# Optimization experiments

Hardware: AMD Instinct MI355X
Metric: run time of the kernel (lower is better)

The kernel has to match this reference:

```python
import jax, jax.numpy as jnp
import numpy as np

D_MODEL = 2048
N_HEADS = 16
N_KV = 4
D_HEAD = D_MODEL // N_HEADS  # 128
N_REP = N_HEADS // N_KV      # 4
ROPE_BASE = 1000000.0


def _rope_tables(T, d_head, dtype):
    # inv_freq = (1/base)^(2i/d) for i in [0, d/2)
    i = jnp.arange(d_head // 2, dtype=jnp.float32)
    inv_freq = (1.0 / ROPE_BASE) ** (2.0 * i / d_head)
    theta = jnp.arange(T, dtype=jnp.float32)[:, None] * inv_freq[None, :]  # [T, d/2]
    theta = jnp.concatenate([theta, theta], axis=-1)                        # [T, d]
    return jnp.sin(theta).astype(dtype), jnp.cos(theta).astype(dtype)


def _apply_rope(x, sin, cos):
    # x: [B, h, T, d]; sin/cos: [T, d]
    x1, x2 = jnp.split(x, 2, axis=-1)
    rot = jnp.concatenate([-x2, x1], axis=-1)
    return cos[None, None] * x + sin[None, None] * rot


def setup_inputs() -> dict:
    key = jax.random.key(0)
    ks = jax.random.split(key, 9)
    B, T = 2, 2048
    s_in = 1.0 / np.sqrt(D_MODEL)
    return {
        "x": jax.random.normal(ks[0], (B, T, D_MODEL), jnp.float32),
        "wq": jax.random.normal(ks[1], (D_MODEL, N_HEADS * D_HEAD), jnp.float32) * s_in,
        "bq": jax.random.normal(ks[2], (N_HEADS * D_HEAD,), jnp.float32) * 0.02,
        "wk": jax.random.normal(ks[3], (D_MODEL, N_KV * D_HEAD), jnp.float32) * s_in,
        "bk": jax.random.normal(ks[4], (N_KV * D_HEAD,), jnp.float32) * 0.02,
        "wv": jax.random.normal(ks[5], (D_MODEL, N_KV * D_HEAD), jnp.float32) * s_in,
        "bv": jax.random.normal(ks[6], (N_KV * D_HEAD,), jnp.float32) * 0.02,
        "wo": jax.random.normal(ks[7], (D_MODEL, D_MODEL), jnp.float32) * s_in,
    }


def reference(x, wq, bq, wk, bk, wv, bv, wo):
    B, T, C = x.shape
    sin, cos = _rope_tables(T, D_HEAD, x.dtype)

    q = (x @ wq + bq).reshape(B, T, N_HEADS, D_HEAD).transpose(0, 2, 1, 3)  # [B,H,T,d]
    k = (x @ wk + bk).reshape(B, T, N_KV, D_HEAD).transpose(0, 2, 1, 3)     # [B,KV,T,d]
    v = (x @ wv + bv).reshape(B, T, N_KV, D_HEAD).transpose(0, 2, 1, 3)     # [B,KV,T,d]

    q = _apply_rope(q, sin, cos)
    k = _apply_rope(k, sin, cos)

    # GQA: group query heads as [B, KV, rep, T, d] to broadcast against k/v
    qg = q.reshape(B, N_KV, N_REP, T, D_HEAD)
    scale = 1.0 / jnp.sqrt(jnp.asarray(D_HEAD, x.dtype))
    scores = jnp.einsum('bkrqd,bksd->bkrqs', qg, k) * scale  # [B,KV,rep,T,S]

    causal = jnp.tril(jnp.ones((T, T), dtype=bool))
    neg = jnp.asarray(jnp.finfo(x.dtype).min, x.dtype)
    scores = jnp.where(causal[None, None, None], scores, neg)
    p = jax.nn.softmax(scores, axis=-1)

    out = jnp.einsum('bkrqs,bksd->bkrqd', p, v)               # [B,KV,rep,T,d]
    out = out.reshape(B, N_HEADS, T, D_HEAD).transpose(0, 2, 1, 3).reshape(B, T, C)
    return out @ wo, k, v
```

## Files before the change

### kernel.cpp

```cpp
#include <hip/hip_runtime.h>
#include <hip/hip_bf16.h>
#include <math.h>

#define BB 2
#define TT 2048
#define DMODEL 2048
#define NH 16
#define NKV 4
#define DH 128
#define NQKV 3072
#define MM (BB*TT)

typedef unsigned short u16;
typedef unsigned int u32;

typedef __bf16 bf16x8 __attribute__((ext_vector_type(8)));
typedef __bf16 bf16x4 __attribute__((ext_vector_type(4)));
typedef short short4v __attribute__((ext_vector_type(4)));
typedef float f32x4 __attribute__((ext_vector_type(4)));

__device__ __forceinline__ u16 f2b(float f) {
  union { float f; u32 u; } v; v.f = f;
  u32 r = v.u + 0x7fffu + ((v.u >> 16) & 1u);
  return (u16)(r >> 16);
}
__device__ __forceinline__ float b2f(u16 h) {
  union { u32 u; float f; } v; v.u = ((u32)h) << 16;
  return v.f;
}
__device__ __forceinline__ u32 pack2bf(float x, float y) {
  union { float f; u32 u; } a, b; a.f = x; b.f = y;
  return ((a.u + 0x8000u) >> 16) | ((b.u + 0x8000u) & 0xffff0000u);
}

__device__ __forceinline__ void gload16(const void* g, void* l) {
  __builtin_amdgcn_global_load_lds(
      (const __attribute__((address_space(1))) unsigned int*)g,
      (__attribute__((address_space(3))) unsigned int*)l, 16, 0, 0);
}

__device__ __forceinline__ float fast_exp2(float x) {
#if __has_builtin(__builtin_amdgcn_exp2f)
  return __builtin_amdgcn_exp2f(x);
#else
  return __expf(x * 0.6931471805599453f);
#endif
}

__device__ __forceinline__ f32x4 mfma16(bf16x4 a, bf16x4 b, f32x4 c) {
#if __has_builtin(__builtin_amdgcn_mfma_f32_16x16x16bf16_1k)
  union { bf16x4 b; short4v s; } ua, ub;
  ua.b = a; ub.b = b;
  return __builtin_amdgcn_mfma_f32_16x16x16bf16_1k(ua.s, ub.s, c, 0, 0, 0);
#elif __has_builtin(__builtin_amdgcn_mfma_f32_16x16x16_bf16)
  return __builtin_amdgcn_mfma_f32_16x16x16_bf16(a, b, c, 0, 0, 0);
#else
  asm volatile("v_mfma_f32_16x16x16_bf16 %0, %1, %2, %0"
               : "+v"(c) : "v"(a), "v"(b));
  return c;
#endif
}

__global__ void cvt_x_kernel(const float* __restrict__ x, u16* __restrict__ xb, int n4) {
  int i = blockIdx.x * 256 + threadIdx.x;
  if (i < n4) {
    float4 v = ((const float4*)x)[i];
    u32 lo = (u32)f2b(v.x) | ((u32)f2b(v.y) << 16);
    u32 hi = (u32)f2b(v.z) | ((u32)f2b(v.w) << 16);
    uint2 r; r.x = lo; r.y = hi;
    ((uint2*)xb)[i] = r;
  }
}

__global__ void rope_table_kernel(float2* __restrict__ tab) {
  int i = blockIdx.x * 256 + threadIdx.x;
  int t = i >> 6, d = i & 63;
  float inv = exp2f(-(float)d * 0.31143075889569023f);
  float th = (float)t * inv;
  float2 cs; cs.x = cosf(th); cs.y = sinf(th);
  tab[i] = cs;
}

__global__ void transpose_cvt_all_kernel(const float* __restrict__ wq,
                                         const float* __restrict__ wk,
                                         const float* __restrict__ wv,
                                         const float* __restrict__ wo,
                                         u16* __restrict__ wqkvT,
                                         u16* __restrict__ woT) {
  __shared__ u16 t[64][65];
  int bx = blockIdx.x;
  const float* src; u16* dst; int srcCols, rowOff, cb;
  if (bx < 32)      { src = wq; dst = wqkvT; srcCols = 2048; rowOff = 0;    cb = bx; }
  else if (bx < 40) { src = wk; dst = wqkvT; srcCols = 512;  rowOff = 2048; cb = bx - 32; }
  else if (bx < 48) { src = wv; dst = wqkvT; srcCols = 512;  rowOff = 2560; cb = bx - 40; }
  else              { src = wo; dst = woT;   srcCols = 2048; rowOff = 0;    cb = bx - 48; }
  int c0 = cb * 64, r0 = blockIdx.y * 64;
  int tid = threadIdx.x;
  for (int i = tid; i < 4096; i += 256) {
    int r = i >> 6, c = i & 63;
    t[r][c] = f2b(src[(size_t)(r0 + r) * srcCols + c0 + c]);
  }
  __syncthreads();
  for (int i = tid; i < 4096; i += 256) {
    int n = i >> 6, k = i & 63;
    dst[(size_t)(rowOff + c0 + n) * 2048 + r0 + k] = t[k][n];
  }
}


#define BARRIER asm volatile("s_barrier" ::: "memory")
#define LGKM0   asm volatile("s_waitcnt lgkmcnt(0)" ::: "memory")

#define STAGE_A(H, KT, RB) do { \
    const u16* g_ = gA + (size_t)(H) * 262144 + (size_t)(KT) * 64; \
    gload16(g_,          sm + (RB) + tid * 8); \
    gload16(g_ + 131072, sm + (RB) + 4096 + tid * 8); \
  } while (0)

#define STAGE_B(H, KT, RB) do { \
    const u16* g_ = gB + (size_t)(H) * 262144 + (size_t)(KT) * 64; \
    gload16(g_,          sm + (RB) + tid * 8); \
    gload16(g_ + 131072, sm + (RB) + 4096 + tid * 8); \
  } while (0)

#define LDA(BU, MH) do { \
    const u16* ab_ = sm + (BU) + (MH) * 8192 + lra * 64; \
    _Pragma("unroll") \
    for (int mi = 0; mi < 4; mi++) { \
      a[mi][0] = *(const bf16x8*)&ab_[mi * 1024 + as0]; \
      a[mi][1] = *(const bf16x8*)&ab_[mi * 1024 + as1]; \
    } \
  } while (0)

#define LDB(BU, NL) do { \
    const u16* bb_ = sm + (BU) + 16384 + hb * 8192 + lrb * 64; \
    _Pragma("unroll") \
    for (int nj = 0; nj < 2; nj++) { \
      b[(NL)*2+nj][0] = *(const bf16x8*)&bb_[((NL)*2+nj) * 1024 + bs0]; \
      b[(NL)*2+nj][1] = *(const bf16x8*)&bb_[((NL)*2+nj) * 1024 + bs1]; \
    } \
  } while (0)

#define MFMAQ(MH, NL) do { \
    _Pragma("unroll") \
    for (int mi = 0; mi < 4; mi++) \
      _Pragma("unroll") \
      for (int nj = 0; nj < 2; nj++) { \
        acc[(MH)*4+mi][(NL)*2+nj] = __builtin_amdgcn_mfma_f32_16x16x32_bf16( \
            a[mi][0], b[(NL)*2+nj][0], acc[(MH)*4+mi][(NL)*2+nj], 0, 0, 0); \
        acc[(MH)*4+mi][(NL)*2+nj] = __builtin_amdgcn_mfma_f32_16x16x32_bf16( \
            a[mi][1], b[(NL)*2+nj][1], acc[(MH)*4+mi][(NL)*2+nj], 0, 0, 0); \
      } \
  } while (0)

#define TILE4(BU, OBU, KA1, KN) do { \
     \
    LDA(BU, 0); LDB(BU, 0); \
    STAGE_A(1, KA1, (OBU) + 8192); \
    asm volatile("s_waitcnt lgkmcnt(8)" ::: "memory"); \
    BARRIER; LGKM0; \
    __builtin_amdgcn_s_setprio(1); MFMAQ(0, 0); __builtin_amdgcn_s_setprio(0); \
    BARRIER; \
     \
    LDB(BU, 1); \
    STAGE_A(0, KN, (BU)); \
    BARRIER; LGKM0; \
    __builtin_amdgcn_s_setprio(1); MFMAQ(0, 1); __builtin_amdgcn_s_setprio(0); \
    BARRIER; \
     \
    LDA(BU, 1); \
    STAGE_B(0, KN, (BU) + 16384); \
    asm volatile("s_waitcnt lgkmcnt(4)" ::: "memory"); \
    BARRIER; LGKM0; \
    __builtin_amdgcn_s_setprio(1); MFMAQ(1, 1); __builtin_amdgcn_s_setprio(0); \
    BARRIER; \
     \
    STAGE_B(1, KN, (BU) + 24576); \
    BARRIER; LGKM0; \
    __builtin_amdgcn_s_setprio(1); MFMAQ(1, 0); __builtin_amdgcn_s_setprio(0); \
    asm volatile("s_waitcnt vmcnt(6)\n\ts_barrier" ::: "memory"); \
  } while (0)

__global__ __launch_bounds__(512, 2) void gemm_qkv_kernel(
    const u16* __restrict__ A, const u16* __restrict__ Bt,
    const float* __restrict__ bq, const float* __restrict__ bk,
    const float* __restrict__ bv, const float2* __restrict__ rtab,
    u16* __restrict__ qb, u16* __restrict__ kb, u16* __restrict__ vt,
    float* __restrict__ outK, float* __restrict__ outV) {
  __shared__ __align__(16) u16 sm[65536];
  const int tid  = threadIdx.x;
  const int lane = tid & 63;
  const int wave = tid >> 6;
  const int wm   = wave >> 2;
  const int wn   = wave & 3;
  const int quad = lane >> 4;
  const int l16  = lane & 15;
  const int m0 = blockIdx.y * 256;
  const int n0 = blockIdx.x * 256;
  const int bx = blockIdx.x;

  const int srow = tid >> 3;
  const int sch  = (tid & 7) ^ (srow & 7);
  const u16* gA = A  + (size_t)(m0 + srow) * 2048 + sch * 8;
  const u16* gB = Bt + (size_t)(n0 + srow) * 2048 + sch * 8;

  const int lra = wm * 64 + l16;
  const int lrb = (wn & 1) * 64 + l16;
  const int hb  = wn >> 1;
  const int as0 = ((quad)     ^ (lra & 7)) << 3;
  const int as1 = ((quad + 4) ^ (lra & 7)) << 3;
  const int bs0 = ((quad)     ^ (lrb & 7)) << 3;
  const int bs1 = ((quad + 4) ^ (lrb & 7)) << 3;

  bf16x8 a[4][2], b[4][2];
  f32x4 acc[8][4];
  const f32x4 zero = {0.f, 0.f, 0.f, 0.f};
#pragma unroll
  for (int i = 0; i < 8; i++)
#pragma unroll
    for (int j = 0; j < 4; j++) acc[i][j] = zero;

  STAGE_A(0, 0, 0);
  STAGE_B(0, 0, 16384);
  STAGE_B(1, 0, 24576);
  STAGE_A(1, 0, 8192);
  STAGE_A(0, 1, 32768);
  STAGE_B(0, 1, 32768 + 16384);
  STAGE_B(1, 1, 32768 + 24576);
  asm volatile("s_waitcnt vmcnt(6)\n\ts_barrier" ::: "memory");

#pragma unroll 1
  for (int it2 = 0; it2 < 16; ++it2) {
    const int ka1 = (2 * it2 + 1) & 31;
    const int kn0 = (2 * it2 + 2) & 31;
    const int kn1 = (2 * it2 + 3) & 31;
    TILE4(0,     32768, ka1, kn0);
    TILE4(32768, 0,     kn0, kn1);
  }

  asm volatile("s_waitcnt vmcnt(0)\n\ts_barrier" ::: "memory");

  const int cls = (bx < 8) ? 0 : ((bx < 10) ? 1 : 2);
#pragma unroll
  for (int nf = 0; nf < 4; nf++) {
    int col = wn * 64 + nf * 16 + l16;
    int gcol = n0 + col;
    float bval = (cls == 0) ? bq[gcol] : ((cls == 1) ? bk[gcol - 2048] : bv[gcol - 2560]);
#pragma unroll
    for (int mh = 0; mh < 2; mh++)
#pragma unroll
      for (int mi = 0; mi < 4; mi++)
#pragma unroll
        for (int r = 0; r < 4; r++) {
          int row = mh * 128 + wm * 64 + mi * 16 + quad * 4 + r;
          int ci = (row * 256 + col) ^ ((row & 7) << 3);
          sm[ci] = f2b(acc[mh * 4 + mi][nf][r] + bval);
        }
  }
  __syncthreads();

  const int bidx = m0 >> 11;
  const int trow0 = m0 & 2047;

  if (cls < 2) {
    const int isQ = (cls == 0);
#pragma unroll
    for (int itq = 0; itq < 8; itq++) {
      int id = tid + itq * 512;
      int lh = id >> 11;
      int rem = id & 2047;
      int row = rem >> 3, oc = rem & 7;
      int t = trow0 + row;
      int rl = t & 63, ttile = t >> 6;
      int sw = (row & 7) << 3;
      int i0 = (row * 256 + lh * 128 + oc * 8);
      uint4 lo = *(const uint4*)&sm[i0 ^ sw];
      uint4 hi = *(const uint4*)&sm[(i0 + 64) ^ sw];
      const u16* plo = (const u16*)&lo;
      const u16* phi = (const u16*)&hi;
      u16 y1[8], y2[8];
      float f1[8], f2v[8];
#pragma unroll
      for (int j = 0; j < 8; j++) {
        float2 cs = rtab[(t << 6) + oc * 8 + j];
        float x1 = b2f(plo[j]), x2 = b2f(phi[j]);
        f1[j]  = cs.x * x1 - cs.y * x2;
        f2v[j] = cs.x * x2 + cs.y * x1;
        y1[j] = f2b(f1[j]);
        y2[j] = f2b(f2v[j]);
      }
      if (isQ) {
        int hh = bx * 2 + lh;
        size_t tb = ((size_t)(bidx * NH + hh) * 32 + ttile) * 8192;
        *(uint4*)&qb[tb + (size_t)((oc)     * 64 + rl) * 8] = *(const uint4*)y1;
        *(uint4*)&qb[tb + (size_t)((oc + 8) * 64 + rl) * 8] = *(const uint4*)y2;
      } else {
        int hh = bx * 2 + lh - 16;
        size_t tb = ((size_t)(bidx * NKV + hh) * 32 + ttile) * 8192;
        *(uint4*)&kb[tb + (size_t)((oc)     * 64 + rl) * 8] = *(const uint4*)y1;
        *(uint4*)&kb[tb + (size_t)((oc + 8) * 64 + rl) * 8] = *(const uint4*)y2;
        size_t base = ((size_t)(bidx * NKV + hh) * TT + t) * DH + oc * 8;
        *(float4*)&outK[base]          = *(const float4*)&f1[0];
        *(float4*)&outK[base + 4]      = *(const float4*)&f1[4];
        *(float4*)&outK[base + 64]     = *(const float4*)&f2v[0];
        *(float4*)&outK[base + 64 + 4] = *(const float4*)&f2v[4];
      }
    }
  } else {
#pragma unroll
    for (int itv = 0; itv < 16; itv++) {
      int id = tid + itv * 512;
      int lh = id >> 12;
      int rem = id & 4095;
      int row = rem >> 4, oc = rem & 15;
      int kvh = bx * 2 + lh - 20;
      int i0 = (row * 256 + lh * 128 + oc * 8) ^ ((row & 7) << 3);
      uint4 v = *(const uint4*)&sm[i0];
      const u16* pv = (const u16*)&v;
      float f[8];
#pragma unroll
      for (int j = 0; j < 8; j++) f[j] = b2f(pv[j]);
      size_t base = ((size_t)(bidx * NKV + kvh) * TT + trow0 + row) * DH + oc * 8;
      *(float4*)&outV[base]     = *(const float4*)&f[0];
      *(float4*)&outV[base + 4] = *(const float4*)&f[4];
    }
#pragma unroll
    for (int itv = 0; itv < 16; itv++) {
      int id = tid + itv * 512;
      int lh = id >> 12;
      int rem = id & 4095;
      int st = rem >> 10;
      int rem2 = rem & 1023;
      int chunk = rem2 >> 7, dl = rem2 & 127;
      int m = chunk >> 2, qd = chunk & 3;
      int kvh = bx * 2 + lh - 20;
      u16 tmp[8];
#pragma unroll
      for (int e = 0; e < 8; e++) {
        int srw = (2 * m + (e >> 2)) * 16 + qd * 4 + (e & 3);
        int row = st * 64 + srw;
        int idx = (row * 256 + lh * 128 + dl) ^ ((row & 7) << 3);
        tmp[e] = sm[idx];
      }
      int tt = (trow0 >> 6) + st;
      size_t tilebase = ((size_t)(bidx * NKV + kvh) * 32 + tt) * 8192;
      *(uint4*)&vt[tilebase + (size_t)(chunk * 128 + dl) * 8] = *(const uint4*)tmp;
    }
  }
}

__global__ __launch_bounds__(256, 3) void gemm_out_kernel(
    const u16* __restrict__ A, const u16* __restrict__ Bt,
    float* __restrict__ Cout, int M, int N, int K) {
  __shared__ __align__(16) u16 smo[16384];
  const int tid  = threadIdx.x;
  const int lane = tid & 63;
  const int wave = tid >> 6;
  const int quad = lane >> 4;
  const int l16  = lane & 15;
  const int m0 = blockIdx.y * 128;
  const int n0 = blockIdx.x * 128;
  const int wrow = (wave >> 1) * 64;
  const int wcol = (wave & 1) * 64;

  f32x4 acc[4][4];
  const f32x4 zero = {0.f, 0.f, 0.f, 0.f};
#pragma unroll
  for (int i = 0; i < 4; i++)
#pragma unroll
    for (int j = 0; j < 4; j++) acc[i][j] = zero;

  const int srow = tid >> 2;
  const int scol = (tid & 3) * 8;
  const u16* ga = A  + (size_t)(m0 + srow) * K + scol;
  const u16* gb = Bt + (size_t)(n0 + srow) * K + scol;

  gload16(ga,                  &smo[tid * 8]);
  gload16(ga + (size_t)64 * K, &smo[2048 + tid * 8]);
  gload16(gb,                  &smo[4096 + tid * 8]);
  gload16(gb + (size_t)64 * K, &smo[6144 + tid * 8]);

  for (int k0 = 0; k0 < K; k0 += 32) {
    const int p = (k0 >> 5) & 1;
    const int kn = (k0 + 32 == K) ? 0 : k0 + 32;
    u16* nb = &smo[(p ^ 1) * 8192];
    gload16(ga + kn,                  nb + tid * 8);
    gload16(ga + kn + (size_t)64 * K, nb + 2048 + tid * 8);
    gload16(gb + kn,                  nb + 4096 + tid * 8);
    gload16(gb + kn + (size_t)64 * K, nb + 6144 + tid * 8);
    asm volatile("s_waitcnt vmcnt(4)\n\ts_barrier" ::: "memory");
    const u16* cb = &smo[p * 8192];
    bf16x8 af[4], bf[4];
#pragma unroll
    for (int mi = 0; mi < 4; mi++)
      af[mi] = *(const bf16x8*)&cb[(wrow + mi * 16 + l16) * 32 + quad * 8];
#pragma unroll
    for (int ni = 0; ni < 4; ni++)
      bf[ni] = *(const bf16x8*)&cb[4096 + (wcol + ni * 16 + l16) * 32 + quad * 8];
    asm volatile("s_waitcnt lgkmcnt(0)\n\ts_barrier" ::: "memory");
#pragma unroll
    for (int mi = 0; mi < 4; mi++)
#pragma unroll
      for (int ni = 0; ni < 4; ni++)
        acc[mi][ni] = __builtin_amdgcn_mfma_f32_16x16x32_bf16(af[mi], bf[ni], acc[mi][ni], 0, 0, 0);
  }
  asm volatile("s_waitcnt vmcnt(0)" ::: "memory");

#pragma unroll
  for (int ni = 0; ni < 4; ni++) {
    int gcol = n0 + wcol + ni * 16 + l16;
#pragma unroll
    for (int mi = 0; mi < 4; mi++) {
#pragma unroll
      for (int r = 0; r < 4; r++) {
        int grow = m0 + wrow + mi * 16 + quad * 4 + r;
        Cout[(size_t)grow * N + gcol] = acc[mi][ni][r];
      }
    }
  }
}

__global__ __launch_bounds__(256, 2) void attn_kernel(
    const u16* __restrict__ Qt, const u16* __restrict__ Kt,
    const u16* __restrict__ Vt, u16* __restrict__ Ob) {
  __shared__ __align__(16) u16 sm[24576];
  u16* vbuf = sm + 16384;

  const int bh = blockIdx.y;
  const int b = bh >> 4, h = bh & 15, kv = h >> 2;
  const int tid = threadIdx.x;
  const int lane = tid & 63;
  const int wave = tid >> 6;
  const int quad = lane >> 4;
  const int l16 = lane & 15;

  const u16* qbase = Qt + (size_t)(b * NH + h) * 32 * 8192;
  const u16* kbase = Kt + (size_t)(b * NKV + kv) * 32 * 8192;
  const u16* vbase = Vt + (size_t)(b * NKV + kv) * 32 * 8192;

  const f32x4 zero = {0.f, 0.f, 0.f, 0.f};
  const float SC2 = 0.08838834764831845f * 1.4426950408889634f;
  const float NEGINF = -__builtin_inff();

  const int x = blockIdx.x;
  const int qt = (x & 1) ? (31 - (x >> 1)) : (x >> 1);
  const int q0 = qt * 64;
  const int qrel = wave * 16 + l16;

  int par = 0;
#pragma unroll
  for (int pp = 0; pp < 4; pp++)
    gload16(kbase + pp * 2048 + tid * 8, sm + pp * 2048 + tid * 8);

  const u16* qtile = qbase + (size_t)qt * 8192;
  bf16x8 qf[4];
#pragma unroll
  for (int kc = 0; kc < 4; kc++)
    qf[kc] = *(const bf16x8*)&qtile[(size_t)((kc * 4 + quad) * 64 + qrel) * 8];

  float mrow = NEGINF, lrow = 0.f;
  f32x4 o[8];
#pragma unroll
  for (int d = 0; d < 8; d++) o[d] = zero;

  for (int kt = 0; kt <= qt; ++kt) {
    u16* kb_c = sm + par * 8192;
    u16* kb_n = sm + (par ^ 1) * 8192;
    const int ktn = (kt < qt) ? kt + 1 : 0;
    const u16* vsrc = vbase + (size_t)kt * 8192;
    const u16* knxt = kbase + (size_t)ktn * 8192;
#pragma unroll
    for (int pp = 0; pp < 4; pp++)
      gload16(vsrc + pp * 2048 + tid * 8, vbuf + pp * 2048 + tid * 8);
#pragma unroll
    for (int pp = 0; pp < 4; pp++)
      gload16(knxt + pp * 2048 + tid * 8, kb_n + pp * 2048 + tid * 8);
    asm volatile("s_waitcnt vmcnt(8)\n\ts_barrier" ::: "memory");

    f32x4 sv[4];
#pragma unroll
    for (int mt = 0; mt < 4; mt++) sv[mt] = zero;
    __builtin_amdgcn_s_setprio(1);
#pragma unroll
    for (int kc = 0; kc < 4; kc++) {
#pragma unroll
      for (int mt = 0; mt < 4; mt++) {
        bf16x8 kf = *(const bf16x8*)&kb_c[(size_t)((kc * 4 + quad) * 64 + mt * 16 + l16) * 8];
        sv[mt] = __builtin_amdgcn_mfma_f32_16x16x32_bf16(kf, qf[kc], sv[mt], 0, 0, 0);
      }
    }
    __builtin_amdgcn_s_setprio(0);

    if (kt == qt) {
#pragma unroll
      for (int mt = 0; mt < 4; mt++)
#pragma unroll
        for (int r = 0; r < 4; r++) {
          int srel = mt * 16 + quad * 4 + r;
          if (srel > qrel) sv[mt][r] = NEGINF;
        }
    }
    float mraw = NEGINF;
#pragma unroll
    for (int mt = 0; mt < 4; mt++)
#pragma unroll
      for (int r = 0; r < 4; r++) mraw = fmaxf(mraw, sv[mt][r]);
    mraw = fmaxf(mraw, __shfl_xor(mraw, 16));
    mraw = fmaxf(mraw, __shfl_xor(mraw, 32));

    bool noresc = __all(mraw <= mrow + 8.0f);
    float mnew = noresc ? mrow : fmaxf(mrow, mraw);
    float msc = mnew * SC2;
    float lsum = 0.f;
#pragma unroll
    for (int mt = 0; mt < 4; mt++) {
#pragma unroll
      for (int r = 0; r < 4; r++) {
        float pe = fast_exp2(__builtin_fmaf(sv[mt][r], SC2, -msc));
        sv[mt][r] = pe;
        lsum += pe;
      }
    }
    if (noresc) {
      lrow += lsum;
    } else {
      float alpha = fast_exp2((mrow - mnew) * SC2);
      mrow = mnew;
      lrow = lrow * alpha + lsum;
#pragma unroll
      for (int dt = 0; dt < 8; dt++) {
        o[dt][0] *= alpha; o[dt][1] *= alpha; o[dt][2] *= alpha; o[dt][3] *= alpha;
      }
    }
    bf16x4 pb[4];
#pragma unroll
    for (int mt = 0; mt < 4; mt++) {
      union { u32 u[2]; bf16x4 v; } pu;
      pu.u[0] = pack2bf(sv[mt][0], sv[mt][1]);
      pu.u[1] = pack2bf(sv[mt][2], sv[mt][3]);
      pb[mt] = pu.v;
    }

    asm volatile("s_waitcnt vmcnt(4)\n\ts_barrier" ::: "memory");
    __builtin_amdgcn_s_setprio(1);
#pragma unroll
    for (int m = 0; m < 2; m++) {
#pragma unroll
      for (int dt = 0; dt < 8; dt++) {
        bf16x8 vf = *(const bf16x8*)&vbuf[(size_t)(((m * 4 + quad) * 128) + dt * 16 + l16) * 8];
        bf16x4 vlo = __builtin_shufflevector(vf, vf, 0, 1, 2, 3);
        bf16x4 vhi = __builtin_shufflevector(vf, vf, 4, 5, 6, 7);
        o[dt] = mfma16(vlo, pb[2 * m],     o[dt]);
        o[dt] = mfma16(vhi, pb[2 * m + 1], o[dt]);
      }
    }
    __builtin_amdgcn_s_setprio(0);
    asm volatile("s_barrier" ::: "memory");
    par ^= 1;
  }

  lrow += __shfl_xor(lrow, 16);
  lrow += __shfl_xor(lrow, 32);
  float inv = 1.0f / lrow;
  int t = q0 + qrel;
  size_t rowbase = (size_t)(b * TT + t) * DMODEL + h * DH;
#pragma unroll
  for (int dt = 0; dt < 8; dt++) {
    uint2 w;
    w.x = pack2bf(o[dt][0] * inv, o[dt][1] * inv);
    w.y = pack2bf(o[dt][2] * inv, o[dt][3] * inv);
    *(uint2*)&Ob[rowbase + dt * 16 + quad * 4] = w;
  }
  asm volatile("s_waitcnt vmcnt(0)" ::: "memory");
}

extern "C" void kernel_launch(void* const* d_in, const int* in_sizes, int n_in,
                              void* d_out, int out_size, void* d_ws, size_t ws_size,
                              hipStream_t stream) {
  (void)in_sizes; (void)n_in; (void)out_size; (void)ws_size;
  const float* x  = (const float*)d_in[0];
  const float* wq = (const float*)d_in[1];
  const float* bq = (const float*)d_in[2];
  const float* wk = (const float*)d_in[3];
  const float* bk = (const float*)d_in[4];
  const float* wv = (const float*)d_in[5];
  const float* bv = (const float*)d_in[6];
  const float* wo = (const float*)d_in[7];
  float* out = (float*)d_out;

  char* ws = (char*)d_ws;
  u16*    xb    = (u16*)(ws);
  u16*    wqkvT = (u16*)(ws + 16777216);
  u16*    woT   = (u16*)(ws + 29360128);
  float2* rtab  = (float2*)(ws + 37748736);
  u16*    qb    = (u16*)(ws + 38797312);
  u16*    kb    = (u16*)(ws + 55574528);
  u16*    vt    = (u16*)(ws + 59768832);
  u16*    ob    = (u16*)(ws + 63963136);

  float* outK = out + (size_t)BB * TT * DMODEL;
  float* outV = outK + (size_t)BB * NKV * TT * DH;

  cvt_x_kernel<<<8192, 256, 0, stream>>>(x, xb, (BB * TT * DMODEL) / 4);
  rope_table_kernel<<<512, 256, 0, stream>>>(rtab);
  transpose_cvt_all_kernel<<<dim3(80, 32), 256, 0, stream>>>(wq, wk, wv, wo, wqkvT, woT);

  gemm_qkv_kernel<<<dim3(NQKV / 256, MM / 256), 512, 0, stream>>>(
      xb, wqkvT, bq, bk, bv, rtab, qb, kb, vt, outK, outV);

  attn_kernel<<<dim3(32, BB * NH), 256, 0, stream>>>(qb, kb, vt, ob);

  gemm_out_kernel<<<dim3(DMODEL / 128, MM / 128), 256, 0, stream>>>(
      ob, woT, out, MM, DMODEL, DMODEL);
}
```

Measured before the change: 330.3 us.

## Double-buffer GEMM fragment registers and pair causal attention tiles per block

```diff
diff --git a/kernel.cpp b/kernel.cpp
--- a/kernel.cpp
+++ b/kernel.cpp
@@ -109,7 +109,6 @@
 
 
 #define BARRIER asm volatile("s_barrier" ::: "memory")
-#define LGKM0   asm volatile("s_waitcnt lgkmcnt(0)" ::: "memory")
 
 #define STAGE_A(H, KT, RB) do { \
     const u16* g_ = gA + (size_t)(H) * 262144 + (size_t)(KT) * 64; \
@@ -123,61 +122,62 @@
     gload16(g_ + 131072, sm + (RB) + 4096 + tid * 8); \
   } while (0)
 
-#define LDA(BU, MH) do { \
+#define LDA2(DST, BU, MH) do { \
     const u16* ab_ = sm + (BU) + (MH) * 8192 + lra * 64; \
     _Pragma("unroll") \
     for (int mi = 0; mi < 4; mi++) { \
-      a[mi][0] = *(const bf16x8*)&ab_[mi * 1024 + as0]; \
-      a[mi][1] = *(const bf16x8*)&ab_[mi * 1024 + as1]; \
+      DST[mi][0] = *(const bf16x8*)&ab_[mi * 1024 + as0]; \
+      DST[mi][1] = *(const bf16x8*)&ab_[mi * 1024 + as1]; \
     } \
   } while (0)
 
-#define LDB(BU, NL) do { \
+#define LDB2(DST, BU, NL) do { \
     const u16* bb_ = sm + (BU) + 16384 + hb * 8192 + lrb * 64; \
     _Pragma("unroll") \
     for (int nj = 0; nj < 2; nj++) { \
-      b[(NL)*2+nj][0] = *(const bf16x8*)&bb_[((NL)*2+nj) * 1024 + bs0]; \
-      b[(NL)*2+nj][1] = *(const bf16x8*)&bb_[((NL)*2+nj) * 1024 + bs1]; \
+      DST[nj][0] = *(const bf16x8*)&bb_[((NL)*2+nj) * 1024 + bs0]; \
+      DST[nj][1] = *(const bf16x8*)&bb_[((NL)*2+nj) * 1024 + bs1]; \
     } \
   } while (0)
 
-#define MFMAQ(MH, NL) do { \
+#define MFMAQ2(AR, BR, MH, NL) do { \
     _Pragma("unroll") \
     for (int mi = 0; mi < 4; mi++) \
       _Pragma("unroll") \
       for (int nj = 0; nj < 2; nj++) { \
         acc[(MH)*4+mi][(NL)*2+nj] = __builtin_amdgcn_mfma_f32_16x16x32_bf16( \
-            a[mi][0], b[(NL)*2+nj][0], acc[(MH)*4+mi][(NL)*2+nj], 0, 0, 0); \
+            AR[mi][0], BR[nj][0], acc[(MH)*4+mi][(NL)*2+nj], 0, 0, 0); \
         acc[(MH)*4+mi][(NL)*2+nj] = __builtin_amdgcn_mfma_f32_16x16x32_bf16( \
-            a[mi][1], b[(NL)*2+nj][1], acc[(MH)*4+mi][(NL)*2+nj], 0, 0, 0); \
+            AR[mi][1], BR[nj][1], acc[(MH)*4+mi][(NL)*2+nj], 0, 0, 0); \
       } \
   } while (0)
 
-#define TILE4(BU, OBU, KA1, KN) do { \
+#define TILE4P(BU, OBU, KA1, KN) do { \
      \
-    LDA(BU, 0); LDB(BU, 0); \
+    LDB2(b23, BU, 1); \
     STAGE_A(1, KA1, (OBU) + 8192); \
-    asm volatile("s_waitcnt lgkmcnt(8)" ::: "memory"); \
-    BARRIER; LGKM0; \
-    __builtin_amdgcn_s_setprio(1); MFMAQ(0, 0); __builtin_amdgcn_s_setprio(0); \
+    BARRIER; \
+    __builtin_amdgcn_s_setprio(1); MFMAQ2(aA, b01, 0, 0); __builtin_amdgcn_s_setprio(0); \
     BARRIER; \
      \
-    LDB(BU, 1); \
+     \
+    LDA2(aB, BU, 1); \
     STAGE_A(0, KN, (BU)); \
-    BARRIER; LGKM0; \
-    __builtin_amdgcn_s_setprio(1); MFMAQ(0, 1); __builtin_amdgcn_s_setprio(0); \
+    BARRIER; \
+    __builtin_amdgcn_s_setprio(1); MFMAQ2(aA, b23, 0, 1); __builtin_amdgcn_s_setprio(0); \
+    asm volatile("s_waitcnt vmcnt(4)\n\ts_barrier" ::: "memory"); \
+     \
+    LDA2(aA, OBU, 0); \
+    STAGE_B(0, KN, (BU) + 16384); \
+    BARRIER; \
+    __builtin_amdgcn_s_setprio(1); MFMAQ2(aB, b01, 1, 0); __builtin_amdgcn_s_setprio(0); \
     BARRIER; \
      \
-    LDA(BU, 1); \
-    STAGE_B(0, KN, (BU) + 16384); \
-    asm volatile("s_waitcnt lgkmcnt(4)" ::: "memory"); \
-    BARRIER; LGKM0; \
-    __builtin_amdgcn_s_setprio(1); MFMAQ(1, 1); __builtin_amdgcn_s_setprio(0); \
+     \
+    LDB2(b01, OBU, 0); \
+    STAGE_B(1, KN, (BU) + 24576); \
     BARRIER; \
-     \
-    STAGE_B(1, KN, (BU) + 24576); \
-    BARRIER; LGKM0; \
-    __builtin_amdgcn_s_setprio(1); MFMAQ(1, 0); __builtin_amdgcn_s_setprio(0); \
+    __builtin_amdgcn_s_setprio(1); MFMAQ2(aB, b23, 1, 1); __builtin_amdgcn_s_setprio(0); \
     asm volatile("s_waitcnt vmcnt(6)\n\ts_barrier" ::: "memory"); \
   } while (0)
 
@@ -212,7 +212,7 @@
   const int bs0 = ((quad)     ^ (lrb & 7)) << 3;
   const int bs1 = ((quad + 4) ^ (lrb & 7)) << 3;
 
-  bf16x8 a[4][2], b[4][2];
+  bf16x8 aA[4][2], aB[4][2], b01[2][2], b23[2][2];
   f32x4 acc[8][4];
   const f32x4 zero = {0.f, 0.f, 0.f, 0.f};
 #pragma unroll
@@ -229,13 +229,16 @@
   STAGE_B(1, 1, 32768 + 24576);
   asm volatile("s_waitcnt vmcnt(6)\n\ts_barrier" ::: "memory");
 
+  LDA2(aA, 0, 0);
+  LDB2(b01, 0, 0);
+
 #pragma unroll 1
   for (int it2 = 0; it2 < 16; ++it2) {
     const int ka1 = (2 * it2 + 1) & 31;
     const int kn0 = (2 * it2 + 2) & 31;
     const int kn1 = (2 * it2 + 3) & 31;
-    TILE4(0,     32768, ka1, kn0);
-    TILE4(32768, 0,     kn0, kn1);
+    TILE4P(0,     32768, ka1, kn0);
+    TILE4P(32768, 0,     kn0, kn1);
   }
 
   asm volatile("s_waitcnt vmcnt(0)\n\ts_barrier" ::: "memory");
@@ -442,134 +445,136 @@
   const float SC2 = 0.08838834764831845f * 1.4426950408889634f;
   const float NEGINF = -__builtin_inff();
 
-  const int x = blockIdx.x;
-  const int qt = (x & 1) ? (31 - (x >> 1)) : (x >> 1);
-  const int q0 = qt * 64;
-  const int qrel = wave * 16 + l16;
-
   int par = 0;
+
 #pragma unroll
   for (int pp = 0; pp < 4; pp++)
     gload16(kbase + pp * 2048 + tid * 8, sm + pp * 2048 + tid * 8);
 
-  const u16* qtile = qbase + (size_t)qt * 8192;
-  bf16x8 qf[4];
-#pragma unroll
-  for (int kc = 0; kc < 4; kc++)
-    qf[kc] = *(const bf16x8*)&qtile[(size_t)((kc * 4 + quad) * 64 + qrel) * 8];
-
-  float mrow = NEGINF, lrow = 0.f;
-  f32x4 o[8];
-#pragma unroll
-  for (int d = 0; d < 8; d++) o[d] = zero;
-
-  for (int kt = 0; kt <= qt; ++kt) {
-    u16* kb_c = sm + par * 8192;
-    u16* kb_n = sm + (par ^ 1) * 8192;
-    const int ktn = (kt < qt) ? kt + 1 : 0;
-    const u16* vsrc = vbase + (size_t)kt * 8192;
-    const u16* knxt = kbase + (size_t)ktn * 8192;
-#pragma unroll
-    for (int pp = 0; pp < 4; pp++)
-      gload16(vsrc + pp * 2048 + tid * 8, vbuf + pp * 2048 + tid * 8);
-#pragma unroll
-    for (int pp = 0; pp < 4; pp++)
-      gload16(knxt + pp * 2048 + tid * 8, kb_n + pp * 2048 + tid * 8);
-    asm volatile("s_waitcnt vmcnt(8)\n\ts_barrier" ::: "memory");
-
-    f32x4 sv[4];
-#pragma unroll
-    for (int mt = 0; mt < 4; mt++) sv[mt] = zero;
-    __builtin_amdgcn_s_setprio(1);
-#pragma unroll
-    for (int kc = 0; kc < 4; kc++) {
+  for (int half = 0; half < 2; ++half) {
+    const int qt = half ? (31 - (int)blockIdx.x) : (int)blockIdx.x;
+    const int q0 = qt * 64;
+    const u16* qtile = qbase + (size_t)qt * 8192;
+    const int qrel = wave * 16 + l16;
+
+    bf16x8 qf[4];
+#pragma unroll
+    for (int kc = 0; kc < 4; kc++)
+      qf[kc] = *(const bf16x8*)&qtile[(size_t)((kc * 4 + quad) * 64 + qrel) * 8];
+
+    float mrow = NEGINF, lrow = 0.f;
+    f32x4 o[8];
+#pragma unroll
+    for (int d = 0; d < 8; d++) o[d] = zero;
+
+    for (int kt = 0; kt <= qt; ++kt) {
+      u16* kb_c = sm + par * 8192;
+      u16* kb_n = sm + (par ^ 1) * 8192;
+      const int ktn = (kt < qt) ? kt + 1 : 0;
+      const u16* vsrc = vbase + (size_t)kt * 8192;
+      const u16* knxt = kbase + (size_t)ktn * 8192;
+#pragma unroll
+      for (int pp = 0; pp < 4; pp++)
+        gload16(vsrc + pp * 2048 + tid * 8, vbuf + pp * 2048 + tid * 8);
+#pragma unroll
+      for (int pp = 0; pp < 4; pp++)
+        gload16(knxt + pp * 2048 + tid * 8, kb_n + pp * 2048 + tid * 8);
+      asm volatile("s_waitcnt vmcnt(8)\n\ts_barrier" ::: "memory");
+
+      f32x4 sv[4];
+#pragma unroll
+      for (int mt = 0; mt < 4; mt++) sv[mt] = zero;
+      __builtin_amdgcn_s_setprio(1);
+#pragma unroll
+      for (int kc = 0; kc < 4; kc++) {
+#pragma unroll
+        for (int mt = 0; mt < 4; mt++) {
+          bf16x8 kf = *(const bf16x8*)&kb_c[(size_t)((kc * 4 + quad) * 64 + mt * 16 + l16) * 8];
+          sv[mt] = __builtin_amdgcn_mfma_f32_16x16x32_bf16(kf, qf[kc], sv[mt], 0, 0, 0);
+        }
+      }
+      __builtin_amdgcn_s_setprio(0);
+
+      if (kt == qt) {
+#pragma unroll
+        for (int mt = 0; mt < 4; mt++)
+#pragma unroll
+          for (int r = 0; r < 4; r++) {
+            int srel = mt * 16 + quad * 4 + r;
+            if (srel > qrel) sv[mt][r] = NEGINF;
+          }
+      }
+      float mraw = NEGINF;
+#pragma unroll
+      for (int mt = 0; mt < 4; mt++)
+#pragma unroll
+        for (int r = 0; r < 4; r++) mraw = fmaxf(mraw, sv[mt][r]);
+      mraw = fmaxf(mraw, __shfl_xor(mraw, 16));
+      mraw = fmaxf(mraw, __shfl_xor(mraw, 32));
+
+      bool noresc = __all(mraw <= mrow + 8.0f);
+      float mnew = noresc ? mrow : fmaxf(mrow, mraw);
+      float msc = mnew * SC2;
+      float lsum = 0.f;
 #pragma unroll
       for (int mt = 0; mt < 4; mt++) {
-        bf16x8 kf = *(const bf16x8*)&kb_c[(size_t)((kc * 4 + quad) * 64 + mt * 16 + l16) * 8];
-        sv[mt] = __builtin_amdgcn_mfma_f32_16x16x32_bf16(kf, qf[kc], sv[mt], 0, 0, 0);
-      }
+#pragma unroll
+        for (int r = 0; r < 4; r++) {
+          float pe = fast_exp2(__builtin_fmaf(sv[mt][r], SC2, -msc));
+          sv[mt][r] = pe;
+          lsum += pe;
+        }
+      }
+      if (noresc) {
+        lrow += lsum;
+      } else {
+        float alpha = fast_exp2((mrow - mnew) * SC2);
+        mrow = mnew;
+        lrow = lrow * alpha + lsum;
+#pragma unroll
+        for (int dt = 0; dt < 8; dt++) {
+          o[dt][0] *= alpha; o[dt][1] *= alpha; o[dt][2] *= alpha; o[dt][3] *= alpha;
+        }
+      }
+      bf16x4 pb[4];
+#pragma unroll
+      for (int mt = 0; mt < 4; mt++) {
+        union { u32 u[2]; bf16x4 v; } pu;
+        pu.u[0] = pack2bf(sv[mt][0], sv[mt][1]);
+        pu.u[1] = pack2bf(sv[mt][2], sv[mt][3]);
+        pb[mt] = pu.v;
+      }
+
+      asm volatile("s_waitcnt vmcnt(4)\n\ts_barrier" ::: "memory");
+      __builtin_amdgcn_s_setprio(1);
+#pragma unroll
+      for (int m = 0; m < 2; m++) {
+#pragma unroll
+        for (int dt = 0; dt < 8; dt++) {
+          bf16x8 vf = *(const bf16x8*)&vbuf[(size_t)(((m * 4 + quad) * 128) + dt * 16 + l16) * 8];
+          bf16x4 vlo = __builtin_shufflevector(vf, vf, 0, 1, 2, 3);
+          bf16x4 vhi = __builtin_shufflevector(vf, vf, 4, 5, 6, 7);
+          o[dt] = mfma16(vlo, pb[2 * m],     o[dt]);
+          o[dt] = mfma16(vhi, pb[2 * m + 1], o[dt]);
+        }
+      }
+      __builtin_amdgcn_s_setprio(0);
+      asm volatile("s_barrier" ::: "memory");
+      par ^= 1;
     }
-    __builtin_amdgcn_s_setprio(0);
-
-    if (kt == qt) {
-#pragma unroll
-      for (int mt = 0; mt < 4; mt++)
-#pragma unroll
-        for (int r = 0; r < 4; r++) {
-          int srel = mt * 16 + quad * 4 + r;
-          if (srel > qrel) sv[mt][r] = NEGINF;
-        }
+
+    lrow += __shfl_xor(lrow, 16);
+    lrow += __shfl_xor(lrow, 32);
+    float inv = 1.0f / lrow;
+    int t = q0 + qrel;
+    size_t rowbase = (size_t)(b * TT + t) * DMODEL + h * DH;
+#pragma unroll
+    for (int dt = 0; dt < 8; dt++) {
+      uint2 w;
+      w.x = pack2bf(o[dt][0] * inv, o[dt][1] * inv);
+      w.y = pack2bf(o[dt][2] * inv, o[dt][3] * inv);
+      *(uint2*)&Ob[rowbase + dt * 16 + quad * 4] = w;
     }
-    float mraw = NEGINF;
-#pragma unroll
-    for (int mt = 0; mt < 4; mt++)
-#pragma unroll
-      for (int r = 0; r < 4; r++) mraw = fmaxf(mraw, sv[mt][r]);
-    mraw = fmaxf(mraw, __shfl_xor(mraw, 16));
-    mraw = fmaxf(mraw, __shfl_xor(mraw, 32));
-
-    bool noresc = __all(mraw <= mrow + 8.0f);
-    float mnew = noresc ? mrow : fmaxf(mrow, mraw);
-    float msc = mnew * SC2;
-    float lsum = 0.f;
-#pragma unroll
-    for (int mt = 0; mt < 4; mt++) {
-#pragma unroll
-      for (int r = 0; r < 4; r++) {
-        float pe = fast_exp2(__builtin_fmaf(sv[mt][r], SC2, -msc));
-        sv[mt][r] = pe;
-        lsum += pe;
-      }
-    }
-    if (noresc) {
-      lrow += lsum;
-    } else {
-      float alpha = fast_exp2((mrow - mnew) * SC2);
-      mrow = mnew;
-      lrow = lrow * alpha + lsum;
-#pragma unroll
-      for (int dt = 0; dt < 8; dt++) {
-        o[dt][0] *= alpha; o[dt][1] *= alpha; o[dt][2] *= alpha; o[dt][3] *= alpha;
-      }
-    }
-    bf16x4 pb[4];
-#pragma unroll
-    for (int mt = 0; mt < 4; mt++) {
-      union { u32 u[2]; bf16x4 v; } pu;
-      pu.u[0] = pack2bf(sv[mt][0], sv[mt][1]);
-      pu.u[1] = pack2bf(sv[mt][2], sv[mt][3]);
-      pb[mt] = pu.v;
-    }
-
-    asm volatile("s_waitcnt vmcnt(4)\n\ts_barrier" ::: "memory");
-    __builtin_amdgcn_s_setprio(1);
-#pragma unroll
-    for (int m = 0; m < 2; m++) {
-#pragma unroll
-      for (int dt = 0; dt < 8; dt++) {
-        bf16x8 vf = *(const bf16x8*)&vbuf[(size_t)(((m * 4 + quad) * 128) + dt * 16 + l16) * 8];
-        bf16x4 vlo = __builtin_shufflevector(vf, vf, 0, 1, 2, 3);
-        bf16x4 vhi = __builtin_shufflevector(vf, vf, 4, 5, 6, 7);
-        o[dt] = mfma16(vlo, pb[2 * m],     o[dt]);
-        o[dt] = mfma16(vhi, pb[2 * m + 1], o[dt]);
-      }
-    }
-    __builtin_amdgcn_s_setprio(0);
-    asm volatile("s_barrier" ::: "memory");
-    par ^= 1;
-  }
-
-  lrow += __shfl_xor(lrow, 16);
-  lrow += __shfl_xor(lrow, 32);
-  float inv = 1.0f / lrow;
-  int t = q0 + qrel;
-  size_t rowbase = (size_t)(b * TT + t) * DMODEL + h * DH;
-#pragma unroll
-  for (int dt = 0; dt < 8; dt++) {
-    uint2 w;
-    w.x = pack2bf(o[dt][0] * inv, o[dt][1] * inv);
-    w.y = pack2bf(o[dt][2] * inv, o[dt][3] * inv);
-    *(uint2*)&Ob[rowbase + dt * 16 + quad * 4] = w;
   }
   asm volatile("s_waitcnt vmcnt(0)" ::: "memory");
 }
@@ -608,7 +613,7 @@
   gemm_qkv_kernel<<<dim3(NQKV / 256, MM / 256), 512, 0, stream>>>(
       xb, wqkvT, bq, bk, bv, rtab, qb, kb, vt, outK, outV);
 
-  attn_kernel<<<dim3(32, BB * NH), 256, 0, stream>>>(qb, kb, vt, ob);
+  attn_kernel<<<dim3(16, BB * NH), 256, 0, stream>>>(qb, kb, vt, ob);
 
   gemm_out_kernel<<<dim3(DMODEL / 128, MM / 128), 256, 0, stream>>>(
       ob, woT, out, MM, DMODEL, DMODEL);
```

Result: faster. 301.2 us (-8.8%).
